# Optimization experiments

Measured on AMD Instinct MI355X. Metric: run time of the kernel, lower is better.

Reference implementation:

```python
import jax, jax.numpy as jnp
import numpy as np

NUM_HEADS = 16
NUM_FEATURES = 1024
HEAD_DIM = NUM_FEATURES // NUM_HEADS
MAX_WAVELENGTH = 10000.0
SCALE_FACTOR = 1.0


def apply_rope(x, positions):
    # x: [B, S, H, D], positions: [B, S]
    half = HEAD_DIM // 2
    fraction = 2.0 * jnp.arange(half, dtype=x.dtype) / HEAD_DIM
    timescale = MAX_WAVELENGTH ** fraction                      # [half]
    sinusoid = positions[..., None].astype(x.dtype) / timescale  # [B, S, half]
    sinusoid = sinusoid[..., None, :] / SCALE_FACTOR             # [B, S, 1, half]
    sin, cos = jnp.sin(sinusoid), jnp.cos(sinusoid)
    x1, x2 = jnp.split(x, 2, axis=-1)
    return jnp.concatenate([x1 * cos - x2 * sin, x2 * cos + x1 * sin], axis=-1).astype(x.dtype)


def setup_inputs() -> dict:
    key = jax.random.key(0)
    ks = jax.random.split(key, 9)
    B, S, F = 2, 2048, NUM_FEATURES
    std = 1.0 / np.sqrt(F)
    inp = {
        "x": jax.random.normal(ks[0], (B, S, F), dtype=jnp.float32),
        "positions": jnp.broadcast_to(jnp.arange(S, dtype=jnp.int32), (B, S)),
        "Wq": jax.random.normal(ks[1], (F, F), dtype=jnp.float32) * std,
        "bq": jnp.zeros((F,), dtype=jnp.float32),
        "Wk": jax.random.normal(ks[2], (F, F), dtype=jnp.float32) * std,
        "bk": jnp.zeros((F,), dtype=jnp.float32),
        "Wv": jax.random.normal(ks[3], (F, F), dtype=jnp.float32) * std,
        "bv": jnp.zeros((F,), dtype=jnp.float32),
        "Wo": jax.random.normal(ks[4], (F, F), dtype=jnp.float32) * std,
        "bo": jnp.zeros((F,), dtype=jnp.float32),
    }
    return inp


def reference(x, positions, Wq, bq, Wk, bk, Wv, bv, Wo, bo):
    B, S, F = x.shape
    H, D = NUM_HEADS, HEAD_DIM
    q = (x @ Wq + bq).reshape(B, S, H, D)
    k = (x @ Wk + bk).reshape(B, S, H, D)
    v = (x @ Wv + bv).reshape(B, S, H, D)
    q = apply_rope(q, positions)
    k = apply_rope(k, positions)
    scale = jnp.sqrt(jnp.asarray(D, dtype=x.dtype))
    # scores: [B, H, S, S]
    scores = jnp.einsum("bqhd,bkhd->bhqk", q, k) / scale
    causal = jnp.tril(jnp.ones((S, S), dtype=bool))
    big_neg = jnp.finfo(scores.dtype).min
    scores = jnp.where(causal, scores, big_neg)
    attn = jax.nn.softmax(scores, axis=-1)
    out = jnp.einsum("bhqk,bkhd->bqhd", attn, v).reshape(B, S, F)
    return out @ Wo + bo
```

## Files before the change

kernel.cpp:

```cpp
#include <hip/hip_runtime.h>
#include <hip/hip_bf16.h>

#define S_LEN 2048
#define NF 1024
#define NH 16
#define HD 64
#define NB 2
#define M_TOT 4096

typedef __bf16 bf16x8 __attribute__((ext_vector_type(8)));
typedef float f32x4 __attribute__((ext_vector_type(4)));
typedef unsigned short u16;

__device__ __forceinline__ u16 f2bf(float f) {
  union { float f; unsigned u; } v; v.f = f;
  unsigned r = v.u + 0x7FFFu + ((v.u >> 16) & 1u);
  return (u16)(r >> 16);
}

__device__ __forceinline__ unsigned pk2bf(float a, float b) {
  __hip_bfloat162 t = __float22bfloat162_rn(make_float2(a, b));
  union { __hip_bfloat162 h; unsigned u; } u; u.h = t; return u.u;
}

__device__ __forceinline__ f32x4 mfma16(bf16x8 a, bf16x8 b, f32x4 c) {
  return __builtin_amdgcn_mfma_f32_16x16x32_bf16(a, b, c, 0, 0, 0);
}

__device__ __forceinline__ void gll16(const u16* g, u16* l) {
  __builtin_amdgcn_global_load_lds(
      (const __attribute__((address_space(1))) unsigned int*)g,
      (__attribute__((address_space(3))) unsigned int*)l, 16, 0, 0);
}

__device__ __forceinline__ u16* swz(u16* base, int row, int chunk) {
  return (u16*)((char*)base + row * 128 + ((chunk ^ (row & 7)) * 16));
}
__device__ __forceinline__ const u16* swz(const u16* base, int row, int chunk) {
  return (const u16*)((const char*)base + row * 128 + ((chunk ^ (row & 7)) * 16));
}

__global__ void __launch_bounds__(256) prep_kernel(
    const float* __restrict__ x, u16* __restrict__ xb,
    const int* __restrict__ positions, float2* __restrict__ rtab,
    const float* __restrict__ W0, const float* __restrict__ W1,
    const float* __restrict__ W2, const float* __restrict__ W3,
    u16* __restrict__ T0, u16* __restrict__ T1,
    u16* __restrict__ T2, u16* __restrict__ T3) {
  __shared__ float t[32][33];
  const int bx = blockIdx.x, tid = threadIdx.x;
  if (bx < 4096) {
    int i = (bx * 256 + tid) * 4;
    float4 v = *(const float4*)(x + i);
    ushort4 o;
    o.x = f2bf(v.x); o.y = f2bf(v.y); o.z = f2bf(v.z); o.w = f2bf(v.w);
    *(ushort4*)(xb + i) = o;
  } else if (bx < 4608) {
    int idx = (bx - 4096) * 256 + tid;
    int p = idx & 31;
    int bs = idx >> 5;
    float pos = (float)positions[bs];
    float ang = pos / __powf(10000.0f, (float)p * (1.0f / 32.0f));
    float sn, cs;
    sincosf(ang, &sn, &cs);
    rtab[idx] = make_float2(sn, cs);
  } else {
    int idx = bx - 4608;
    int z = idx >> 10, rem = idx & 1023;
    const float* W = (z == 0) ? W0 : (z == 1) ? W1 : (z == 2) ? W2 : W3;
    u16* Wt = (z == 0) ? T0 : (z == 1) ? T1 : (z == 2) ? T2 : T3;
    int n0 = (rem & 31) * 32, k0 = (rem >> 5) * 32;
    int tx = tid & 31, ty0 = tid >> 5;
#pragma unroll
    for (int i = 0; i < 4; i++) {
      int ty = ty0 + i * 8;
      t[ty][tx] = W[(size_t)(k0 + ty) * NF + n0 + tx];
    }
    __syncthreads();
#pragma unroll
    for (int i = 0; i < 4; i++) {
      int ty = ty0 + i * 8;
      Wt[(size_t)(n0 + ty) * NF + k0 + tx] = f2bf(t[tx][ty]);
    }
  }
}

__device__ __forceinline__ void mm_core(const u16* __restrict__ A, const u16* __restrict__ Bt,
                                        int m0, int n0, int kstart,
                                        u16* As, u16* Bs, f32x4 acc[4][4]) {
  const int tid = threadIdx.x;
  const int lane = tid & 63, w = tid >> 6;
  const int l15 = lane & 15, quad = lane >> 4;
  const int wr = w >> 1, wc = w & 1;
#pragma unroll
  for (int i = 0; i < 4; i++)
#pragma unroll
    for (int j = 0; j < 4; j++) {
      f32x4 z = {0.f, 0.f, 0.f, 0.f};
      acc[i][j] = z;
    }
  const u16* gA[4];
  const u16* gB[4];
#pragma unroll
  for (int i = 0; i < 4; i++) {
    int ci = i * 256 + tid;
    int row = ci >> 3, col = (ci & 7) ^ (row & 7);
    gA[i] = &A[(size_t)(m0 + row) * NF + col * 8];
    gB[i] = &Bt[(size_t)(n0 + row) * NF + col * 8];
  }
  for (int s = 0; s < NF / 64; s++) {
    const int k0 = ((s + kstart) & (NF / 64 - 1)) * 64;
    __syncthreads();
#pragma unroll
    for (int i = 0; i < 4; i++) {
      gll16(gA[i] + k0, &As[(i * 256 + w * 64) * 8]);
      gll16(gB[i] + k0, &Bs[(i * 256 + w * 64) * 8]);
    }
    __syncthreads();
#pragma unroll
    for (int kk = 0; kk < 2; kk++) {
      bf16x8 af[4], bfr[4];
#pragma unroll
      for (int i = 0; i < 4; i++)
        af[i] = *(const bf16x8*)swz(As, wr * 64 + i * 16 + l15, kk * 4 + quad);
#pragma unroll
      for (int j = 0; j < 4; j++)
        bfr[j] = *(const bf16x8*)swz(Bs, wc * 64 + j * 16 + l15, kk * 4 + quad);
#pragma unroll
      for (int i = 0; i < 4; i++)
#pragma unroll
        for (int j = 0; j < 4; j++)
          acc[i][j] = mfma16(af[i], bfr[j], acc[i][j]);
    }
  }
}

__device__ __forceinline__ void mm_core64(const u16* __restrict__ A, const u16* __restrict__ Bt,
                                          int m0, int n0, int kstart,
                                          u16* As, u16* Bs, f32x4 acc[2][4]) {
  const int tid = threadIdx.x;
  const int lane = tid & 63, w = tid >> 6;
  const int l15 = lane & 15, quad = lane >> 4;
  const int wr = w >> 1, wc = w & 1;
#pragma unroll
  for (int i = 0; i < 2; i++)
#pragma unroll
    for (int j = 0; j < 4; j++) {
      f32x4 z = {0.f, 0.f, 0.f, 0.f};
      acc[i][j] = z;
    }
  const u16* gA[2];
  const u16* gB[4];
#pragma unroll
  for (int i = 0; i < 2; i++) {
    int ci = i * 256 + tid;
    int row = ci >> 3, col = (ci & 7) ^ (row & 7);
    gA[i] = &A[(size_t)(m0 + row) * NF + col * 8];
  }
#pragma unroll
  for (int i = 0; i < 4; i++) {
    int ci = i * 256 + tid;
    int row = ci >> 3, col = (ci & 7) ^ (row & 7);
    gB[i] = &Bt[(size_t)(n0 + row) * NF + col * 8];
  }
  for (int s = 0; s < NF / 64; s++) {
    const int k0 = ((s + kstart) & (NF / 64 - 1)) * 64;
    __syncthreads();
#pragma unroll
    for (int i = 0; i < 2; i++)
      gll16(gA[i] + k0, &As[(i * 256 + w * 64) * 8]);
#pragma unroll
    for (int i = 0; i < 4; i++)
      gll16(gB[i] + k0, &Bs[(i * 256 + w * 64) * 8]);
    __syncthreads();
#pragma unroll
    for (int kk = 0; kk < 2; kk++) {
      bf16x8 af[2], bfr[4];
#pragma unroll
      for (int i = 0; i < 2; i++)
        af[i] = *(const bf16x8*)swz(As, wr * 32 + i * 16 + l15, kk * 4 + quad);
#pragma unroll
      for (int j = 0; j < 4; j++)
        bfr[j] = *(const bf16x8*)swz(Bs, wc * 64 + j * 16 + l15, kk * 4 + quad);
#pragma unroll
      for (int i = 0; i < 2; i++)
#pragma unroll
        for (int j = 0; j < 4; j++)
          acc[i][j] = mfma16(af[i], bfr[j], acc[i][j]);
    }
  }
}

#define QSCL 0.18033688f

__global__ void __launch_bounds__(256) gemm_qkv_kernel(
    const u16* __restrict__ xb,
    const u16* __restrict__ wtq, const u16* __restrict__ wtk, const u16* __restrict__ wtv,
    const float* __restrict__ bq, const float* __restrict__ bk, const float* __restrict__ bv,
    const float2* __restrict__ rtab,
    u16* __restrict__ qo, u16* __restrict__ ko, u16* __restrict__ vto) {
  __shared__ u16 As[128 * 64], Bs[128 * 64];
  const int bx = blockIdx.x;
  const int xcd = bx & 7, slot = bx >> 3;
  const int z = slot >> 5, intra = slot & 31;
  const int by = (xcd >> 1) * 8 + (intra >> 2);
  const int bxn = (xcd & 1) * 4 + (intra & 3);
  const int kstart = (intra * 3 + z * 5) & 15;
  const u16* Wt = (z == 0) ? wtq : (z == 1) ? wtk : wtv;
  const float* bias = (z == 0) ? bq : (z == 1) ? bk : bv;
  const int m0 = by * 128, n0 = bxn * 128;
  f32x4 acc[4][4];
  mm_core(xb, Wt, m0, n0, kstart, As, Bs, acc);
  const int tid = threadIdx.x;
  const int lane = tid & 63, w = tid >> 6;
  const int l15 = lane & 15, quad = lane >> 4;
  const int wr = w >> 1, wc = w & 1;
  if (z < 2) {
    u16* out = (z == 0) ? qo : ko;
    const float oscl = (z == 0) ? QSCL : 1.0f;
#pragma unroll
    for (int i = 0; i < 4; i++) {
#pragma unroll
      for (int r = 0; r < 4; r++) {
        int gm = m0 + wr * 64 + i * 16 + quad * 4 + r;
        int b = gm >> 11, s = gm & 2047;
#pragma unroll
        for (int j = 0; j < 2; j++) {
          int col1 = n0 + wc * 64 + j * 16 + l15;
          int p = j * 16 + l15;
          float2 sc = rtab[gm * 32 + p];
          float x1 = acc[i][j][r] + bias[col1];
          float x2 = acc[i][j + 2][r] + bias[col1 + 32];
          float o1 = (x1 * sc.y - x2 * sc.x) * oscl;
          float o2 = (x2 * sc.y + x1 * sc.x) * oscl;
          int h = col1 >> 6;
          size_t base = ((size_t)((b * NH + h) * S_LEN + s)) * HD;
          out[base + p] = f2bf(o1);
          out[base + p + 32] = f2bf(o2);
        }
      }
    }
  } else {
#pragma unroll
    for (int i = 0; i < 4; i++) {
      int gm0 = m0 + wr * 64 + i * 16 + quad * 4;
      int b = gm0 >> 11, s0 = gm0 & 2047;
#pragma unroll
      for (int j = 0; j < 4; j++) {
        int col = n0 + wc * 64 + j * 16 + l15;
        int h = col >> 6, d = col & 63;
        float bb = bias[col];
        ushort4 pk;
        pk.x = f2bf(acc[i][j][0] + bb);
        pk.y = f2bf(acc[i][j][1] + bb);
        pk.z = f2bf(acc[i][j][2] + bb);
        pk.w = f2bf(acc[i][j][3] + bb);
        *(ushort4*)&vto[((size_t)((b * NH + h) * HD + d)) * S_LEN + s0] = pk;
      }
    }
  }
}

__global__ void __launch_bounds__(256) gemm_o_kernel(const u16* __restrict__ ab,
                                                     const u16* __restrict__ wto,
                                                     const float* __restrict__ bo,
                                                     float* __restrict__ out) {
  __shared__ u16 As[64 * 64], Bs[128 * 64];
  const int bxr = blockIdx.x;
  const int xcd = bxr & 7, intra = bxr >> 3;
  const int by = xcd * 8 + (intra >> 3);
  const int bxn = intra & 7;
  const int kstart = (intra * 3) & 15;
  const int m0 = by * 64, n0 = bxn * 128;
  f32x4 acc[2][4];
  mm_core64(ab, wto, m0, n0, kstart, As, Bs, acc);
  const int tid = threadIdx.x;
  const int lane = tid & 63, w = tid >> 6;
  const int l15 = lane & 15, quad = lane >> 4;
  const int wr = w >> 1, wc = w & 1;
#pragma unroll
  for (int i = 0; i < 2; i++) {
#pragma unroll
    for (int j = 0; j < 4; j++) {
      int col = n0 + wc * 64 + j * 16 + l15;
      float bb = bo[col];
#pragma unroll
      for (int r = 0; r < 4; r++) {
        int gm = m0 + wr * 32 + i * 16 + quad * 4 + r;
        out[(size_t)gm * NF + col] = acc[i][j][r] + bb;
      }
    }
  }
}

__global__ void __launch_bounds__(256) attn_kernel(
    const u16* __restrict__ qb, const u16* __restrict__ kb,
    const u16* __restrict__ vtb, u16* __restrict__ ob) {
  __shared__ u16 ks[2 * 64 * 64];
  __shared__ u16 vs[2 * 64 * 64];
  __shared__ u16 ps[4][16 * 64];
  const int bx = blockIdx.x;
  const int qt = (bx < 512) ? (31 - (bx >> 5)) : ((bx - 512) >> 5);
  const int bh = bx & 31;
  const int tid = threadIdx.x;
  const int lane = tid & 63, w = tid >> 6, l15 = lane & 15, quad = lane >> 4;
  const int bb = bh >> 4, h = bh & 15;
  const size_t kvbase = (size_t)bh * S_LEN;
  const size_t vbase = (size_t)bh * HD;
  const int Q0 = qt * 64;
  const int nit = qt + 1;

  size_t kSrc[2], vSrc[2];
  int dstOff[2];
#pragma unroll
  for (int i = 0; i < 2; i++) {
    int ci = i * 256 + w * 64 + lane;
    int kr = ci >> 3, kc = ci & 7;
    kSrc[i] = (kvbase + kr) * HD + ((kc ^ (kr & 7)) * 8);
    vSrc[i] = (vbase + kr) * S_LEN + ((kc ^ (kr & 7)) * 8);
    dstOff[i] = (i * 256 + w * 64) * 8;
  }

  bf16x8 ones;
#pragma unroll
  for (int i = 0; i < 8; i++) ones[i] = (__bf16)1.0f;

  bf16x8 qf[2];
  {
    const u16* qrow = &qb[(kvbase + Q0 + w * 16 + l15) * HD];
#pragma unroll
    for (int hh = 0; hh < 2; hh++)
      qf[hh] = *(const bf16x8*)&qrow[hh * 32 + quad * 8];
  }

  float mrun = -1e30f;
  f32x4 Oa[4], lacc;
  { f32x4 z = {0.f, 0.f, 0.f, 0.f}; lacc = z;
#pragma unroll
    for (int t = 0; t < 4; t++) Oa[t] = z; }

#pragma unroll
  for (int i = 0; i < 2; i++) {
    gll16(&kb[kSrc[i]], ks + dstOff[i]);
    gll16(&vtb[vSrc[i]], vs + dstOff[i]);
  }
  __syncthreads();

  int cur = 0;
  for (int it = 0; it < nit; ++it) {
    const int k0 = it * 64;
    const bool pf = (it + 1 < nit);
    u16* ksc = ks + cur * 4096;
    u16* vsc = vs + cur * 4096;
    if (pf) {
      int k1 = k0 + 64;
      u16* ksn = ks + (cur ^ 1) * 4096;
      u16* vsn = vs + (cur ^ 1) * 4096;
#pragma unroll
      for (int i = 0; i < 2; i++) {
        gll16(&kb[kSrc[i] + (size_t)k1 * HD], ksn + dstOff[i]);
        gll16(&vtb[vSrc[i] + k1], vsn + dstOff[i]);
      }
    }
    f32x4 sf[4];
#pragma unroll
    for (int t = 0; t < 4; t++) {
      bf16x8 ak0 = *(const bf16x8*)swz(ksc, t * 16 + l15, quad);
      bf16x8 ak1 = *(const bf16x8*)swz(ksc, t * 16 + l15, 4 + quad);
      f32x4 z = {0.f, 0.f, 0.f, 0.f};
      z = mfma16(ak0, qf[0], z);
      z = mfma16(ak1, qf[1], z);
      sf[t] = z;
    }
    if (it == qt) {
      int qg = Q0 + w * 16 + l15;
#pragma unroll
      for (int t = 0; t < 4; t++)
#pragma unroll
        for (int rr = 0; rr < 4; rr++)
          if (k0 + t * 16 + quad * 4 + rr > qg) sf[t][rr] = -1e30f;
    }
    float alph;
    {
      float mx = sf[0][0];
#pragma unroll
      for (int t = 0; t < 4; t++)
#pragma unroll
        for (int rr = 0; rr < 4; rr++) mx = fmaxf(mx, sf[t][rr]);
      mx = fmaxf(mx, __shfl_xor(mx, 16, 64));
      mx = fmaxf(mx, __shfl_xor(mx, 32, 64));
      float mnew = fmaxf(mrun, mx);
      alph = __builtin_amdgcn_exp2f(mrun - mnew);
      mrun = mnew;
#pragma unroll
      for (int t = 0; t < 4; t++)
#pragma unroll
        for (int rr = 0; rr < 4; rr++)
          sf[t][rr] = __builtin_amdgcn_exp2f(sf[t][rr] - mnew);
    }
    if (__any(alph < 1.f)) {
#pragma unroll
      for (int rr = 0; rr < 4; rr++) {
        float ao = __shfl(alph, quad * 4 + rr, 64);
#pragma unroll
        for (int t = 0; t < 4; t++) Oa[t][rr] *= ao;
        lacc[rr] *= ao;
      }
    }
#pragma unroll
    for (int t = 0; t < 4; t++) {
      uint2 pkk;
      pkk.x = pk2bf(sf[t][0], sf[t][1]);
      pkk.y = pk2bf(sf[t][2], sf[t][3]);
      int chnk = 2 * t + (quad >> 1);
      *(uint2*)((char*)ps[w] + l15 * 128 + ((chnk ^ (l15 & 7)) * 16) + (quad & 1) * 8) = pkk;
    }
    __builtin_amdgcn_wave_barrier();
    bf16x8 ap[2];
#pragma unroll
    for (int hh = 0; hh < 2; hh++)
      ap[hh] = *(const bf16x8*)swz(ps[w], l15, hh * 4 + quad);
#pragma unroll
    for (int t = 0; t < 4; t++) {
      bf16x8 bv0 = *(const bf16x8*)swz(vsc, t * 16 + l15, quad);
      bf16x8 bv1 = *(const bf16x8*)swz(vsc, t * 16 + l15, 4 + quad);
      Oa[t] = mfma16(ap[0], bv0, Oa[t]);
      Oa[t] = mfma16(ap[1], bv1, Oa[t]);
    }
    lacc = mfma16(ap[0], ones, lacc);
    lacc = mfma16(ap[1], ones, lacc);
    if (pf) {
      __syncthreads();
      cur ^= 1;
    }
  }

#pragma unroll
  for (int rr = 0; rr < 4; rr++) {
    float inv = 1.f / lacc[rr];
    int qg = Q0 + w * 16 + quad * 4 + rr;
    size_t rowb = ((size_t)(bb * S_LEN + qg)) * NF + h * HD;
#pragma unroll
    for (int t = 0; t < 4; t++)
      ob[rowb + t * 16 + l15] = f2bf(Oa[t][rr] * inv);
  }
}

extern "C" void kernel_launch(void* const* d_in, const int* in_sizes, int n_in,
                              void* d_out, int out_size, void* d_ws, size_t ws_size,
                              hipStream_t stream) {
  const float* x  = (const float*)d_in[0];
  const int* pos  = (const int*)d_in[1];
  const float* Wq = (const float*)d_in[2];
  const float* bq = (const float*)d_in[3];
  const float* Wk = (const float*)d_in[4];
  const float* bk = (const float*)d_in[5];
  const float* Wv = (const float*)d_in[6];
  const float* bv = (const float*)d_in[7];
  const float* Wo = (const float*)d_in[8];
  const float* bo = (const float*)d_in[9];
  float* out = (float*)d_out;

  u16* xb  = (u16*)d_ws;
  u16* wtq = xb + (size_t)M_TOT * NF;
  u16* wtk = wtq + (size_t)NF * NF;
  u16* wtv = wtk + (size_t)NF * NF;
  u16* wto = wtv + (size_t)NF * NF;
  u16* qb  = wto + (size_t)NF * NF;
  u16* kb  = qb + (size_t)M_TOT * NF;
  u16* vtb = kb + (size_t)M_TOT * NF;
  float2* rtab = (float2*)(vtb + (size_t)M_TOT * NF);
  u16* attnb = xb;

  prep_kernel<<<dim3(8704), 256, 0, stream>>>(x, xb, pos, rtab,
                                              Wq, Wk, Wv, Wo, wtq, wtk, wtv, wto);
  gemm_qkv_kernel<<<dim3(768), 256, 0, stream>>>(xb, wtq, wtk, wtv, bq, bk, bv,
                                                 rtab, qb, kb, vtb);
  attn_kernel<<<dim3(1024), 256, 0, stream>>>(qb, kb, vtb, attnb);
  gemm_o_kernel<<<dim3(512), 256, 0, stream>>>(attnb, wto, bo, out);
}
```

Baseline: 194.2 us.

## Split attention into 32-row query tiles with 2-wave blocks, drop double buffering

The attention kernel now uses 128-thread blocks that each handle 32 query rows, launching twice as many blocks in longest-first order. K/V double buffering is removed: each iteration loads a single 64-key tile, synchronises, computes, and synchronises again. The intent is finer load balancing across the causal triangle and lower LDS use per block for higher occupancy. The cost is that global-to-LDS loads no longer overlap compute, and each K/V tile is loaded by twice as many blocks.

```diff
diff --git a/kernel.cpp b/kernel.cpp
--- a/kernel.cpp
+++ b/kernel.cpp
@@ -293,33 +293,34 @@
   }
 }
 
-__global__ void __launch_bounds__(256) attn_kernel(
+__global__ void __launch_bounds__(128) attn_kernel(
     const u16* __restrict__ qb, const u16* __restrict__ kb,
     const u16* __restrict__ vtb, u16* __restrict__ ob) {
-  __shared__ u16 ks[2 * 64 * 64];
-  __shared__ u16 vs[2 * 64 * 64];
-  __shared__ u16 ps[4][16 * 64];
+  __shared__ u16 ks[64 * 64];
+  __shared__ u16 vs[64 * 64];
+  __shared__ u16 ps[2][16 * 64];
   const int bx = blockIdx.x;
-  const int qt = (bx < 512) ? (31 - (bx >> 5)) : ((bx - 512) >> 5);
+  const int qt = 63 - (bx >> 5);
   const int bh = bx & 31;
   const int tid = threadIdx.x;
   const int lane = tid & 63, w = tid >> 6, l15 = lane & 15, quad = lane >> 4;
   const int bb = bh >> 4, h = bh & 15;
   const size_t kvbase = (size_t)bh * S_LEN;
-  const size_t vbase = (size_t)bh * HD;
-  const int Q0 = qt * 64;
-  const int nit = qt + 1;
-
-  size_t kSrc[2], vSrc[2];
-  int dstOff[2];
-#pragma unroll
-  for (int i = 0; i < 2; i++) {
-    int ci = i * 256 + w * 64 + lane;
+  const int Q0 = qt * 32;
+  const int nit = (qt >> 1) + 1;
+
+  unsigned kSrc[4], vSrc[4];
+  int dstOff[4];
+#pragma unroll
+  for (int i = 0; i < 4; i++) {
+    int ci = i * 128 + tid;
     int kr = ci >> 3, kc = ci & 7;
-    kSrc[i] = (kvbase + kr) * HD + ((kc ^ (kr & 7)) * 8);
-    vSrc[i] = (vbase + kr) * S_LEN + ((kc ^ (kr & 7)) * 8);
-    dstOff[i] = (i * 256 + w * 64) * 8;
-  }
+    kSrc[i] = (unsigned)((kr)*HD + ((kc ^ (kr & 7)) * 8));
+    vSrc[i] = (unsigned)((kr)*S_LEN + ((kc ^ (kr & 7)) * 8));
+    dstOff[i] = (i * 128 + w * 64) * 8;
+  }
+  const u16* kbb = kb + kvbase * HD;
+  const u16* vtbb = vtb + (size_t)bh * HD * S_LEN;
 
   bf16x8 ones;
 #pragma unroll
@@ -339,40 +340,25 @@
 #pragma unroll
     for (int t = 0; t < 4; t++) Oa[t] = z; }
 
-#pragma unroll
-  for (int i = 0; i < 2; i++) {
-    gll16(&kb[kSrc[i]], ks + dstOff[i]);
-    gll16(&vtb[vSrc[i]], vs + dstOff[i]);
-  }
-  __syncthreads();
-
-  int cur = 0;
   for (int it = 0; it < nit; ++it) {
     const int k0 = it * 64;
-    const bool pf = (it + 1 < nit);
-    u16* ksc = ks + cur * 4096;
-    u16* vsc = vs + cur * 4096;
-    if (pf) {
-      int k1 = k0 + 64;
-      u16* ksn = ks + (cur ^ 1) * 4096;
-      u16* vsn = vs + (cur ^ 1) * 4096;
-#pragma unroll
-      for (int i = 0; i < 2; i++) {
-        gll16(&kb[kSrc[i] + (size_t)k1 * HD], ksn + dstOff[i]);
-        gll16(&vtb[vSrc[i] + k1], vsn + dstOff[i]);
-      }
-    }
+#pragma unroll
+    for (int i = 0; i < 4; i++) {
+      gll16(&kbb[(size_t)k0 * HD + kSrc[i]], ks + dstOff[i]);
+      gll16(&vtbb[(size_t)k0 + vSrc[i]], vs + dstOff[i]);
+    }
+    __syncthreads();
     f32x4 sf[4];
 #pragma unroll
     for (int t = 0; t < 4; t++) {
-      bf16x8 ak0 = *(const bf16x8*)swz(ksc, t * 16 + l15, quad);
-      bf16x8 ak1 = *(const bf16x8*)swz(ksc, t * 16 + l15, 4 + quad);
+      bf16x8 ak0 = *(const bf16x8*)swz(ks, t * 16 + l15, quad);
+      bf16x8 ak1 = *(const bf16x8*)swz(ks, t * 16 + l15, 4 + quad);
       f32x4 z = {0.f, 0.f, 0.f, 0.f};
       z = mfma16(ak0, qf[0], z);
       z = mfma16(ak1, qf[1], z);
       sf[t] = z;
     }
-    if (it == qt) {
+    if (it == nit - 1) {
       int qg = Q0 + w * 16 + l15;
 #pragma unroll
       for (int t = 0; t < 4; t++)
@@ -422,17 +408,14 @@
       ap[hh] = *(const bf16x8*)swz(ps[w], l15, hh * 4 + quad);
 #pragma unroll
     for (int t = 0; t < 4; t++) {
-      bf16x8 bv0 = *(const bf16x8*)swz(vsc, t * 16 + l15, quad);
-      bf16x8 bv1 = *(const bf16x8*)swz(vsc, t * 16 + l15, 4 + quad);
+      bf16x8 bv0 = *(const bf16x8*)swz(vs, t * 16 + l15, quad);
+      bf16x8 bv1 = *(const bf16x8*)swz(vs, t * 16 + l15, 4 + quad);
       Oa[t] = mfma16(ap[0], bv0, Oa[t]);
       Oa[t] = mfma16(ap[1], bv1, Oa[t]);
     }
     lacc = mfma16(ap[0], ones, lacc);
     lacc = mfma16(ap[1], ones, lacc);
-    if (pf) {
-      __syncthreads();
-      cur ^= 1;
-    }
+    __syncthreads();
   }
 
 #pragma unroll
@@ -476,6 +459,6 @@
                                               Wq, Wk, Wv, Wo, wtq, wtk, wtv, wto);
   gemm_qkv_kernel<<<dim3(768), 256, 0, stream>>>(xb, wtq, wtk, wtv, bq, bk, bv,
                                                  rtab, qb, kb, vtb);
-  attn_kernel<<<dim3(1024), 256, 0, stream>>>(qb, kb, vtb, attnb);
+  attn_kernel<<<dim3(2048), 128, 0, stream>>>(qb, kb, vtb, attnb);
   gemm_o_kernel<<<dim3(512), 256, 0, stream>>>(attnb, wto, bo, out);
 }
```

Result: slower. 198.6 us (+2.3%).
